# Optimization experiments

Measured on AMD Instinct MI355X. Metric: run time of the kernel, lower is better.

## Reference

```python
import jax, jax.numpy as jnp
import numpy as np

DIM = 384
HEADS = 12
K = 3          # kernel_size
PAD = 1
STRIDE = 1
B, H, W = 8, 56, 56


def conv1x1(x, w, b=None):
    # x: [B,C,H,W], w: [O,C]
    y = jnp.einsum('bchw,oc->bohw', x, w)
    if b is not None:
        y = y + b[None, :, None, None]
    return y


def unfold(x, k, p, s):
    # torch nn.Unfold: returns patches [B, C, k*k, nH, nW], kernel row-major, channel-major overall
    Bx, C, Hx, Wx = x.shape
    nH = (Hx + 2 * p - k) // s + 1
    nW = (Wx + 2 * p - k) // s + 1
    xp = jnp.pad(x, ((0, 0), (0, 0), (p, p), (p, p)))
    cols = [xp[:, :, i:i + s * nH:s, j:j + s * nW:s] for i in range(k) for j in range(k)]
    return jnp.stack(cols, axis=2), nH, nW


def fold(col, Hx, Wx, k, p, s):
    # torch F.fold (col2im): scatter-add overlapping windows. col: [B, C, k*k, nH, nW]
    Bx, C, _, nH, nW = col.shape
    canvas = jnp.zeros((Bx, C, Hx + 2 * p, Wx + 2 * p), col.dtype)
    idx = 0
    for i in range(k):
        for j in range(k):
            canvas = canvas.at[:, :, i:i + s * nH:s, j:j + s * nW:s].add(col[:, :, idx])
            idx += 1
    return canvas[:, :, p:p + Hx, p:p + Wx]


def setup_inputs() -> dict:
    key = jax.random.key(0)
    ks = jax.random.split(key, 5)
    k2 = K * K
    x = jax.random.normal(ks[0], (B, DIM, H, W), dtype=jnp.float32)
    v_w = jax.random.normal(ks[1], (DIM, DIM), dtype=jnp.float32) * 0.02
    v_b = jnp.zeros((DIM,), dtype=jnp.float32)
    attn_w = jax.random.normal(ks[2], (k2 * k2 * HEADS, DIM), dtype=jnp.float32) * 0.02
    proj_w = jax.random.normal(ks[3], (DIM, DIM), dtype=jnp.float32) * 0.02
    return {'x': x, 'v_w': v_w, 'v_b': v_b, 'attn_w': attn_w, 'proj_w': proj_w}


def reference(x, v_w, v_b, attn_w, proj_w):
    Bx, C, Hx, Wx = x.shape
    k2 = K * K
    hd = C // HEADS  # head dim
    # value projection + unfold into overlapping k x k windows
    v = conv1x1(x, v_w, v_b)
    vcol, nH, nW = unfold(v, K, PAD, STRIDE)        # [B, C, k2, nH, nW]
    L = nH * nW
    v = vcol.reshape(Bx, HEADS, hd, k2, L)          # split C = (heads, hd), heads slow
    v = v.transpose(0, 1, 4, 3, 2)                  # [B, n, L, k2(d), hd]
    # adaptive avg pool to (nH, nW); with stride=1 this is identity (pool window 1)
    ph, pw = Hx // nH, Wx // nW
    xp = x.reshape(Bx, C, nH, ph, nW, pw).mean(axis=(3, 5))
    # per-pixel attention logits, channel layout = ((i*k2 + d)*HEADS + head)
    a = jnp.einsum('bchw,oc->bohw', xp, attn_w)     # [B, k2*k2*n, nH, nW]
    a = a.reshape(Bx, k2, k2, HEADS, L)             # [B, i, d, n, L]
    a = a.transpose(0, 3, 4, 1, 2)                  # [B, n, L, i, d]
    a = jax.nn.softmax(a, axis=-1)
    out = jnp.einsum('bnlid,bnldh->bnlih', a, v)    # [B, n, L, i, hd]
    out = out.transpose(0, 1, 4, 3, 2)              # [B, n, hd, i, L] -> channel (n*hd+h)
    out = out.reshape(Bx, C, k2, nH, nW)
    out = fold(out, Hx, Wx, K, PAD, STRIDE)         # scatter-add windows back
    return conv1x1(out, proj_w)
```

## Files before the change

kernel.cpp:

```cpp
#include <hip/hip_runtime.h>
#include <hip/hip_bf16.h>

#define DIM   384
#define HEADS 12
#define K2    9
#define HH    56
#define WW    56
#define HWP   3136
#define BB    8
#define AO    972
#define AOP   1024
#define MCAT  1408
#define PP    3200

typedef __hip_bfloat16 bf16;
typedef short bf16x8 __attribute__((ext_vector_type(8)));
typedef short bf16x4v __attribute__((ext_vector_type(4)));
typedef float f32x4 __attribute__((ext_vector_type(4)));

static __device__ __forceinline__ float b2f(bf16 v) { return __bfloat162float(v); }
static __device__ __forceinline__ float bs2f(short s) {
    return __uint_as_float(((unsigned int)(unsigned short)s) << 16);
}
static __device__ __forceinline__ short f2bs(float f) {
    __hip_bfloat16 h = __float2bfloat16(f);
    return *(short*)&h;
}

static __device__ __forceinline__ void gl_lds16(const bf16* g, bf16* l) {
    __builtin_amdgcn_global_load_lds(
        (const __attribute__((address_space(1))) unsigned int*)g,
        (__attribute__((address_space(3))) unsigned int*)l, 16, 0, 0);
}

__global__ __launch_bounds__(256) void xpose_kernel(
        const float* __restrict__ x, bf16* __restrict__ xT) {
    const int lane = threadIdx.x & 63, w = threadIdx.x >> 6;
    const int p = blockIdx.x * 64 + lane;
    const int b = blockIdx.y;
    bf16* dst = xT + ((size_t)b * PP + p) * DIM;
    if (p >= HWP) {
        bf16x8 z = {};
        for (int cg = w; cg < 48; cg += 4) *(bf16x8*)(dst + cg * 8) = z;
        return;
    }
    const float* src = x + (size_t)b * DIM * HWP + p;
    for (int cg = w; cg < 48; cg += 4) {
        bf16x8 v;
#pragma unroll
        for (int j = 0; j < 8; j++) v[j] = f2bs(src[(size_t)(cg * 8 + j) * HWP]);
        *(bf16x8*)(dst + cg * 8) = v;
    }
}

__global__ __launch_bounds__(256) void wconv_kernel(
        const float* __restrict__ src, bf16* __restrict__ dst, int rows, int rows_pad) {
    int idx = blockIdx.x * 256 + threadIdx.x;
    if (idx >= rows_pad * DIM) return;
    float v = (idx < rows * DIM) ? src[idx] : 0.f;
    *(short*)&dst[idx] = f2bs(v);
}

#define GEMM_MAIN_LOOP(Ab, Bb, lA, lB, acc)                                    \
    for (int k0 = 0; k0 < DIM; k0 += 32) {                                     \
        _Pragma("unroll")                                                      \
        for (int r = 0; r < 2; r++) {                                          \
            int idx = r * 256 + t;                                             \
            gl_lds16(Ab + (size_t)(idx >> 2) * DIM + k0 + (idx & 3) * 8,       \
                     lA + idx * 8);                                            \
        }                                                                      \
        _Pragma("unroll")                                                      \
        for (int r = 0; r < 2; r++) {                                          \
            int idx = r * 256 + t;                                             \
            gl_lds16(Bb + (size_t)(idx >> 2) * DIM + k0 + (idx & 3) * 8,       \
                     lB + idx * 8);                                            \
        }                                                                      \
        __syncthreads();                                                       \
        bf16x8 af[4], bfr[4];                                                  \
        _Pragma("unroll")                                                      \
        for (int mt = 0; mt < 4; mt++)                                         \
            af[mt] = *(const bf16x8*)(lA + (wm * 64 + mt * 16 + l16) * 32 + quad * 8); \
        _Pragma("unroll")                                                      \
        for (int nt = 0; nt < 4; nt++)                                         \
            bfr[nt] = *(const bf16x8*)(lB + (wn * 64 + nt * 16 + l16) * 32 + quad * 8); \
        _Pragma("unroll")                                                      \
        for (int mt = 0; mt < 4; mt++)                                         \
            _Pragma("unroll")                                                  \
            for (int nt = 0; nt < 4; nt++)                                     \
                acc[mt][nt] = __builtin_amdgcn_mfma_f32_16x16x32_bf16(         \
                    af[mt], bfr[nt], acc[mt][nt], 0, 0, 0);                    \
        __syncthreads();                                                       \
    }

__global__ __launch_bounds__(256) void gemm12_kernel(
        const bf16* __restrict__ A, const bf16* __restrict__ Bt,
        const float* __restrict__ bias, bf16* __restrict__ vT,
        bf16* __restrict__ lT) {
    __shared__ bf16 lds[8192];
    bf16* lA = lds;
    bf16* lB = lds + 4096;
    const int t = threadIdx.x;
    const int lane = t & 63, w = t >> 6;
    const int wm = w & 1, wn = w >> 1;
    const int quad = lane >> 4, l16 = lane & 15;
    const int n0 = blockIdx.x * 128;
    const int m0 = blockIdx.y * 128;
    const int b = blockIdx.z;

    const bf16* Ab = A + (size_t)m0 * DIM;
    const bf16* Bb = Bt + ((size_t)b * PP + n0) * DIM;

    f32x4 acc[4][4] = {};
    GEMM_MAIN_LOOP(Ab, Bb, lA, lB, acc)

    const bool isv = (m0 < 384);
    bf16* outp = isv ? vT : lT;
    const int ostr = isv ? DIM : AOP;
    const int ch0 = isv ? m0 : m0 - 384;

    bf16* wbuf = lds + w * 1152;
#pragma unroll
    for (int nt = 0; nt < 4; nt++) {
#pragma unroll
        for (int mt = 0; mt < 4; mt++) {
            float4 bi = make_float4(0.f, 0.f, 0.f, 0.f);
            if (isv) bi = *(const float4*)(bias + ch0 + wm * 64 + mt * 16 + quad * 4);
            bf16x4v pk;
            pk[0] = f2bs(acc[mt][nt][0] + bi.x);
            pk[1] = f2bs(acc[mt][nt][1] + bi.y);
            pk[2] = f2bs(acc[mt][nt][2] + bi.z);
            pk[3] = f2bs(acc[mt][nt][3] + bi.w);
            *(bf16x4v*)(wbuf + l16 * 72 + mt * 16 + quad * 4) = pk;
        }
        __syncthreads();
        int nr = lane >> 2;
        int mc = (lane & 3) * 16;
        bf16x8 v0 = *(const bf16x8*)(wbuf + nr * 72 + mc);
        bf16x8 v1 = *(const bf16x8*)(wbuf + nr * 72 + mc + 8);
        int p = n0 + wn * 64 + nt * 16 + nr;
        if (p < HWP) {
            bf16* dp = outp + ((size_t)b * PP + p) * ostr + ch0 + wm * 64 + mc;
            *(bf16x8*)dp = v0;
            *(bf16x8*)(dp + 8) = v1;
        }
        __syncthreads();
    }
}

__global__ __launch_bounds__(256) void gemm_planar_kernel(
        const bf16* __restrict__ A, const bf16* __restrict__ Bt,
        float* __restrict__ out) {
    __shared__ bf16 lds[8192];
    bf16* lA = lds;
    bf16* lB = lds + 4096;
    const int t = threadIdx.x;
    const int lane = t & 63, w = t >> 6;
    const int wm = w & 1, wn = w >> 1;
    const int quad = lane >> 4, l16 = lane & 15;
    const int n0 = blockIdx.x * 128;
    const int m0 = blockIdx.y * 128;
    const int b = blockIdx.z;

    const bf16* Ab = A + (size_t)m0 * DIM;
    const bf16* Bb = Bt + ((size_t)b * PP + n0) * DIM;

    f32x4 acc[4][4] = {};
    GEMM_MAIN_LOOP(Ab, Bb, lA, lB, acc)

#pragma unroll
    for (int mt = 0; mt < 4; mt++) {
#pragma unroll
        for (int nt = 0; nt < 4; nt++) {
            int p = n0 + wn * 64 + nt * 16 + l16;
            if (p >= HWP) continue;
#pragma unroll
            for (int reg = 0; reg < 4; reg++) {
                int o = m0 + wm * 64 + mt * 16 + quad * 4 + reg;
                out[((size_t)b * DIM + o) * HWP + p] = acc[mt][nt][reg];
            }
        }
    }
}

__global__ __launch_bounds__(384) void attn_fold_kernel(
        const bf16* __restrict__ lT, const bf16* __restrict__ vT,
        bf16* __restrict__ cT) {
    __shared__ bf16 P[8 * 9 * 12 * 9];
    __shared__ float Wf[8 * 25 * 12];
    const int t = threadIdx.x;
    const int b = blockIdx.y;
    const int pix0 = blockIdx.x * 8;
    const int Y = pix0 / WW, X0 = pix0 % WW;

    for (int r = t; r < 864; r += 384) {
        const int px = r / 108, rem = r % 108;
        const int i = rem / 12, n = rem % 12;
        const int ir = i / 3, ic = i % 3;
        const int yi = Y + 1 - ir, xi = X0 + px + 1 - ic;
        bf16* Pd = &P[r * 9];
        if (yi < 0 || yi >= HH || xi < 0 || xi >= WW) {
#pragma unroll
            for (int d = 0; d < K2; d++) *(short*)&Pd[d] = 0;
        } else {
            const bf16* base = lT + ((size_t)b * PP + yi * WW + xi) * AOP + i * 108 + n;
            float lv[K2];
            float m = -1e30f;
#pragma unroll
            for (int d = 0; d < K2; d++) {
                lv[d] = b2f(base[d * 12]);
                m = fmaxf(m, lv[d]);
            }
            float s = 0.f;
#pragma unroll
            for (int d = 0; d < K2; d++) { lv[d] = __expf(lv[d] - m); s += lv[d]; }
            const float inv = 1.f / s;
#pragma unroll
            for (int d = 0; d < K2; d++) *(short*)&Pd[d] = f2bs(lv[d] * inv);
        }
    }
    __syncthreads();

    for (int e = t; e < 2400; e += 384) {
        const int px = e / 300, rem = e % 300;
        const int off = rem / 12, n = rem % 12;
        const int dy = off / 5 - 2, dx = off % 5 - 2;
        const int ir_lo = max(0, -dy), ir_hi = min(2, 2 - dy);
        const int ic_lo = max(0, -dx), ic_hi = min(2, 2 - dx);
        float wsum = 0.f;
        for (int ir = ir_lo; ir <= ir_hi; ir++)
            for (int ic = ic_lo; ic <= ic_hi; ic++) {
                const int i = ir * 3 + ic;
                const int d = (dy + ir) * 3 + (dx + ic);
                wsum += b2f(P[((px * 9 + i) * 12 + n) * 9 + d]);
            }
        Wf[e] = wsum;
    }
    __syncthreads();

    const int px = t / 48, cg = t % 48;
    const int X = X0 + px;
    const int n = cg >> 2;
    const float* Wp = &Wf[px * 300];
    const bf16* vb = vT + (size_t)b * PP * DIM;
    float acc[8] = {};
#pragma unroll
    for (int dy = -2; dy <= 2; dy++) {
        const int ny = Y + dy;
        if (ny < 0 || ny >= HH) continue;
#pragma unroll
        for (int dx = -2; dx <= 2; dx++) {
            const int nx = X + dx;
            const bool ok = (nx >= 0 && nx < WW);
            const int nxc = min(max(nx, 0), WW - 1);
            const float w = ok ? Wp[((dy + 2) * 5 + dx + 2) * 12 + n] : 0.f;
            bf16x8 vv = *(const bf16x8*)(vb + (size_t)(ny * WW + nxc) * DIM + cg * 8);
#pragma unroll
            for (int j = 0; j < 8; j++) acc[j] += w * bs2f(vv[j]);
        }
    }
    bf16x8 po;
#pragma unroll
    for (int j = 0; j < 8; j++) po[j] = f2bs(acc[j]);
    *(bf16x8*)(cT + ((size_t)b * PP + pix0 + px) * DIM + cg * 8) = po;
}

extern "C" void kernel_launch(void* const* d_in, const int* in_sizes, int n_in,
                              void* d_out, int out_size, void* d_ws, size_t ws_size,
                              hipStream_t stream) {
    const float* x      = (const float*)d_in[0];
    const float* v_w    = (const float*)d_in[1];
    const float* v_b    = (const float*)d_in[2];
    const float* attn_w = (const float*)d_in[3];
    const float* proj_w = (const float*)d_in[4];
    float* out = (float*)d_out;

    bf16* xT    = (bf16*)d_ws;
    bf16* vT    = xT + (size_t)BB * PP * DIM;
    bf16* lT    = vT + (size_t)BB * PP * DIM;
    bf16* wcat  = lT + (size_t)BB * PP * AOP;
    bf16* wp    = wcat + (size_t)MCAT * DIM;
    bf16* cT    = xT;

    wconv_kernel<<<(384 * DIM + 255) / 256, 256, 0, stream>>>(v_w, wcat, 384, 384);
    wconv_kernel<<<(1024 * DIM + 255) / 256, 256, 0, stream>>>(attn_w, wcat + 384 * DIM, AO, 1024);
    wconv_kernel<<<(384 * DIM + 255) / 256, 256, 0, stream>>>(proj_w, wp, 384, 384);
    xpose_kernel<<<dim3(PP / 64, BB), 256, 0, stream>>>(x, xT);

    gemm12_kernel<<<dim3(PP / 128, MCAT / 128, BB), 256, 0, stream>>>(wcat, xT, v_b, vT, lT);
    attn_fold_kernel<<<dim3(HWP / 8, BB), 384, 0, stream>>>(lT, vT, cT);
    gemm_planar_kernel<<<dim3(PP / 128, 3, BB), 256, 0, stream>>>(wp, cT, out);
}
```

Baseline: 228.3 us.

## Load GEMM A-fragments directly from global, swizzle B tile LDS, merge weight conversions

The GEMM main loop now reads the weight (A) fragments straight from global memory into registers instead of staging them through LDS. The B tile in LDS uses a rotated k-quad swizzle to cut bank conflicts. The epilogue of gemm12 gets its own LDS staging buffer, so the per-tile __syncthreads calls go away because each wave only touches its own region. The three weight-conversion launches are merged into one. The A loads now depend on L2/L1 hits for the small weight matrices and their latency is no longer hidden by the LDS staging.

```diff
diff --git a/kernel.cpp b/kernel.cpp
--- a/kernel.cpp
+++ b/kernel.cpp
@@ -53,36 +53,46 @@
     }
 }
 
-__global__ __launch_bounds__(256) void wconv_kernel(
-        const float* __restrict__ src, bf16* __restrict__ dst, int rows, int rows_pad) {
-    int idx = blockIdx.x * 256 + threadIdx.x;
-    if (idx >= rows_pad * DIM) return;
-    float v = (idx < rows * DIM) ? src[idx] : 0.f;
-    *(short*)&dst[idx] = f2bs(v);
-}
-
-#define GEMM_MAIN_LOOP(Ab, Bb, lA, lB, acc)                                    \
+__global__ __launch_bounds__(256) void wconv_all_kernel(
+        const float* __restrict__ v_w, const float* __restrict__ attn_w,
+        const float* __restrict__ proj_w, bf16* __restrict__ wcat,
+        bf16* __restrict__ wp) {
+    const int idx = blockIdx.x * 256 + threadIdx.x;
+    const int NCAT = MCAT * DIM;
+    if (idx < NCAT) {
+        const int row = idx / DIM, col = idx % DIM;
+        float v;
+        if (row < 384) v = v_w[row * DIM + col];
+        else { const int r2 = row - 384; v = (r2 < AO) ? attn_w[r2 * DIM + col] : 0.f; }
+        *(short*)&wcat[idx] = f2bs(v);
+    } else {
+        const int j = idx - NCAT;
+        if (j < 384 * DIM) *(short*)&wp[j] = f2bs(proj_w[j]);
+    }
+}
+
+#define GEMM_MAIN_LOOP_V2(Ab, Bb, lB, acc)                                     \
+    {                                                                          \
+    const int swz = ((quad + (l16 >> 1)) & 3) * 8;                             \
     for (int k0 = 0; k0 < DIM; k0 += 32) {                                     \
         _Pragma("unroll")                                                      \
         for (int r = 0; r < 2; r++) {                                          \
             int idx = r * 256 + t;                                             \
-            gl_lds16(Ab + (size_t)(idx >> 2) * DIM + k0 + (idx & 3) * 8,       \
-                     lA + idx * 8);                                            \
+            int row = idx >> 2;                                                \
+            int kq = ((idx & 3) - (idx >> 3)) & 3;                             \
+            gl_lds16(Bb + (size_t)row * DIM + k0 + kq * 8, lB + idx * 8);      \
         }                                                                      \
-        _Pragma("unroll")                                                      \
-        for (int r = 0; r < 2; r++) {                                          \
-            int idx = r * 256 + t;                                             \
-            gl_lds16(Bb + (size_t)(idx >> 2) * DIM + k0 + (idx & 3) * 8,       \
-                     lB + idx * 8);                                            \
-        }                                                                      \
+        bf16x8 af[4];                                                          \
+        _Pragma("unroll")                                                      \
+        for (int mt = 0; mt < 4; mt++)                                         \
+            af[mt] = *(const bf16x8*)(Ab +                                     \
+                (size_t)(wm * 64 + mt * 16 + l16) * DIM + k0 + quad * 8);      \
         __syncthreads();                                                       \
-        bf16x8 af[4], bfr[4];                                                  \
-        _Pragma("unroll")                                                      \
-        for (int mt = 0; mt < 4; mt++)                                         \
-            af[mt] = *(const bf16x8*)(lA + (wm * 64 + mt * 16 + l16) * 32 + quad * 8); \
+        bf16x8 bfr[4];                                                         \
         _Pragma("unroll")                                                      \
         for (int nt = 0; nt < 4; nt++)                                         \
-            bfr[nt] = *(const bf16x8*)(lB + (wn * 64 + nt * 16 + l16) * 32 + quad * 8); \
+            bfr[nt] = *(const bf16x8*)(lB +                                    \
+                (wn * 64 + nt * 16 + l16) * 32 + swz);                         \
         _Pragma("unroll")                                                      \
         for (int mt = 0; mt < 4; mt++)                                         \
             _Pragma("unroll")                                                  \
@@ -90,15 +100,15 @@
                 acc[mt][nt] = __builtin_amdgcn_mfma_f32_16x16x32_bf16(         \
                     af[mt], bfr[nt], acc[mt][nt], 0, 0, 0);                    \
         __syncthreads();                                                       \
+    }                                                                          \
     }
 
 __global__ __launch_bounds__(256) void gemm12_kernel(
         const bf16* __restrict__ A, const bf16* __restrict__ Bt,
         const float* __restrict__ bias, bf16* __restrict__ vT,
         bf16* __restrict__ lT) {
-    __shared__ bf16 lds[8192];
-    bf16* lA = lds;
-    bf16* lB = lds + 4096;
+    __shared__ bf16 lB[4096];
+    __shared__ bf16 wrep[4 * 1152];
     const int t = threadIdx.x;
     const int lane = t & 63, w = t >> 6;
     const int wm = w & 1, wn = w >> 1;
@@ -111,14 +121,16 @@
     const bf16* Bb = Bt + ((size_t)b * PP + n0) * DIM;
 
     f32x4 acc[4][4] = {};
-    GEMM_MAIN_LOOP(Ab, Bb, lA, lB, acc)
+    GEMM_MAIN_LOOP_V2(Ab, Bb, lB, acc)
 
     const bool isv = (m0 < 384);
     bf16* outp = isv ? vT : lT;
     const int ostr = isv ? DIM : AOP;
     const int ch0 = isv ? m0 : m0 - 384;
 
-    bf16* wbuf = lds + w * 1152;
+    bf16* wbuf = wrep + w * 1152;
+    const int nr = lane >> 2;
+    const int mc = (lane & 3) * 16;
 #pragma unroll
     for (int nt = 0; nt < 4; nt++) {
 #pragma unroll
@@ -132,27 +144,21 @@
             pk[3] = f2bs(acc[mt][nt][3] + bi.w);
             *(bf16x4v*)(wbuf + l16 * 72 + mt * 16 + quad * 4) = pk;
         }
-        __syncthreads();
-        int nr = lane >> 2;
-        int mc = (lane & 3) * 16;
         bf16x8 v0 = *(const bf16x8*)(wbuf + nr * 72 + mc);
         bf16x8 v1 = *(const bf16x8*)(wbuf + nr * 72 + mc + 8);
-        int p = n0 + wn * 64 + nt * 16 + nr;
+        const int p = n0 + wn * 64 + nt * 16 + nr;
         if (p < HWP) {
             bf16* dp = outp + ((size_t)b * PP + p) * ostr + ch0 + wm * 64 + mc;
             *(bf16x8*)dp = v0;
             *(bf16x8*)(dp + 8) = v1;
         }
-        __syncthreads();
     }
 }
 
 __global__ __launch_bounds__(256) void gemm_planar_kernel(
         const bf16* __restrict__ A, const bf16* __restrict__ Bt,
         float* __restrict__ out) {
-    __shared__ bf16 lds[8192];
-    bf16* lA = lds;
-    bf16* lB = lds + 4096;
+    __shared__ bf16 lB[4096];
     const int t = threadIdx.x;
     const int lane = t & 63, w = t >> 6;
     const int wm = w & 1, wn = w >> 1;
@@ -165,7 +171,7 @@
     const bf16* Bb = Bt + ((size_t)b * PP + n0) * DIM;
 
     f32x4 acc[4][4] = {};
-    GEMM_MAIN_LOOP(Ab, Bb, lA, lB, acc)
+    GEMM_MAIN_LOOP_V2(Ab, Bb, lB, acc)
 
 #pragma unroll
     for (int mt = 0; mt < 4; mt++) {
@@ -281,9 +287,8 @@
     bf16* wp    = wcat + (size_t)MCAT * DIM;
     bf16* cT    = xT;
 
-    wconv_kernel<<<(384 * DIM + 255) / 256, 256, 0, stream>>>(v_w, wcat, 384, 384);
-    wconv_kernel<<<(1024 * DIM + 255) / 256, 256, 0, stream>>>(attn_w, wcat + 384 * DIM, AO, 1024);
-    wconv_kernel<<<(384 * DIM + 255) / 256, 256, 0, stream>>>(proj_w, wp, 384, 384);
+    const int NW = MCAT * DIM + 384 * DIM;
+    wconv_all_kernel<<<(NW + 255) / 256, 256, 0, stream>>>(v_w, attn_w, proj_w, wcat, wp);
     xpose_kernel<<<dim3(PP / 64, BB), 256, 0, stream>>>(x, xT);
 
     gemm12_kernel<<<dim3(PP / 128, MCAT / 128, BB), 256, 0, stream>>>(wcat, xT, v_b, vT, lT);
```

New measurement: 258.5 us. 1.13x slower.
